# Optimization experiments

Hardware: AMD Instinct MI355X
Metric: run time of the kernel (lower is better)

Reference implementation:

```python
import jax, jax.numpy as jnp
import numpy as np

N_HEADS = 4
D_HEAD = 64
SCALE = D_HEAD ** -0.5


def setup_inputs() -> dict:
    key = jax.random.key(0)
    k0, k1, k2, k3, k4 = jax.random.split(key, 5)
    C = 256
    return {
        "x": jax.random.normal(k0, (32, C, 32, 32), dtype=jnp.float32),
        "W_qkv": jax.random.normal(k1, (C, 3 * N_HEADS * D_HEAD), dtype=jnp.float32) * 0.02,
        "b_qkv": jax.random.normal(k2, (3 * N_HEADS * D_HEAD,), dtype=jnp.float32) * 0.02,
        "W_out": jax.random.normal(k3, (C, C), dtype=jnp.float32) * 0.02,
        "b_out": jax.random.normal(k4, (C,), dtype=jnp.float32) * 0.02,
    }


def reference(x, W_qkv, b_qkv, W_out, b_out):
    b, c, h, w = x.shape
    # [B, C, H, W] -> [B, S, C], S = H*W  (NOTE: GroupNorm is defined in the
    # original module but never applied in forward; we match that exactly.)
    xs = x.reshape(b, c, h * w).transpose(0, 2, 1)
    qkv = (xs @ W_qkv + b_qkv).reshape(b, -1, N_HEADS, 3 * D_HEAD)
    q, k, v = jnp.split(qkv, 3, axis=-1)  # each [B, S, H, D]
    scores = jnp.einsum('bihd,bjhd->bijh', q, k) * SCALE  # [B, S, S, H]
    attn = jax.nn.softmax(scores, axis=2)  # softmax over key index j
    res = jnp.einsum('bijh,bjhd->bihd', attn, v).reshape(b, -1, N_HEADS * D_HEAD)
    res = res @ W_out + b_out + xs
    return res.transpose(0, 2, 1).reshape(b, c, h, w)
```

## Files before the change

### kernel.cpp

```cpp
#include <hip/hip_runtime.h>

#define NH 4
#define DH 64
#define SS 1024
#define CC 256

typedef __attribute__((ext_vector_type(8))) short short8;
typedef __attribute__((ext_vector_type(4))) float floatx4;
typedef __attribute__((ext_vector_type(16))) float floatx16;
typedef __attribute__((ext_vector_type(2))) unsigned uint2v;

#define MFMA16(a, b, c) __builtin_amdgcn_mfma_f32_16x16x32_bf16(a, b, c, 0, 0, 0)
#define MFMA32(a, b, c) __builtin_amdgcn_mfma_f32_32x32x16_bf16(a, b, c, 0, 0, 0)

#define QSCALE 0.18033688011112042f

__device__ __forceinline__ short f2bf(float f) {
    union { float f; unsigned u; } v; v.f = f;
    unsigned r = (v.u + 0x7fffu + ((v.u >> 16) & 1u)) >> 16;
    return (short)r;
}
__device__ __forceinline__ unsigned bfrn(float f) {
    union { float f; unsigned u; } v; v.f = f;
    return (v.u + 0x7fffu + ((v.u >> 16) & 1u)) >> 16;
}
__device__ __forceinline__ unsigned pk2_trunc(float a, float b) {
    union { float f; unsigned u; } ua, ub; ua.f = a; ub.f = b;
    return (ua.u >> 16) | (ub.u & 0xFFFF0000u);
}
__device__ __forceinline__ unsigned pk2_rn(float a, float b) {
    return bfrn(a) | (bfrn(b) << 16);
}

__global__ __launch_bounds__(256) void k_prep(const float* __restrict__ x,
                                              const float* __restrict__ Wqkv,
                                              const float* __restrict__ Wout,
                                              short* __restrict__ xs,
                                              short* __restrict__ Wqkv_t,
                                              short* __restrict__ Wout_t) {
    int bid = blockIdx.x;
    if (bid < 2048) {
        __shared__ float tile[64][65];
        int b = bid >> 6;
        int s0 = ((bid >> 2) & 15) * 64;
        int c0 = (bid & 3) * 64;
        int t = threadIdx.x;
        int tx = t & 63, ty = t >> 6;
        for (int i = 0; i < 16; ++i) {
            int c = ty + i * 4;
            tile[tx][c] = x[((b * CC) + (c0 + c)) * SS + s0 + tx];
        }
        __syncthreads();
        for (int i = 0; i < 8; ++i) {
            int s = (t >> 5) + i * 8;
            int cp = (t & 31) * 2;
            short2 v;
            v.x = f2bf(tile[s][cp]);
            v.y = f2bf(tile[s][cp + 1]);
            *(short2*)(&xs[((b * SS) + (s0 + s)) * CC + c0 + cp]) = v;
        }
    } else {
        int idx = (bid - 2048) * 256 + threadIdx.x;
        if (idx < 768 * 256) {
            int n = idx >> 8, k = idx & 255;
            Wqkv_t[idx] = f2bf(Wqkv[k * 768 + n]);
        } else {
            int j = idx - 768 * 256;
            int c = j >> 8, k = j & 255;
            Wout_t[j] = f2bf(Wout[k * 256 + c]);
        }
    }
}

__global__ __launch_bounds__(256) void k_qkv(const short* __restrict__ xs,
                                             const short* __restrict__ Wt,
                                             const float* __restrict__ bqkv,
                                             short* __restrict__ qtw,
                                             short* __restrict__ kw,
                                             short* __restrict__ vtw) {
    __shared__ short smem[10240];
    short* As = smem;
    short* Bs = smem + 5120;
    int bid = blockIdx.x;
    int idx = bid >> 3;
    int m0 = ((bid & 7) * 32 + idx / 6) * 128;
    int n0 = (idx % 6) * 128;
    int t = threadIdx.x;
    int lane = t & 63, wid = t >> 6;
    int wr = wid >> 1, wc = wid & 1;
    int c16 = lane & 15, qd = lane >> 4;

    floatx4 acc[4][4] = {};
    short8 pa[2], pb[2];

    for (int j = 0; j < 2; ++j) {
        int id = j * 256 + t, row = id >> 2, cc = id & 3;
        pa[j] = *(const short8*)(&xs[(m0 + row) * CC + cc * 8]);
        pb[j] = *(const short8*)(&Wt[(n0 + row) * CC + cc * 8]);
    }
    for (int kt = 0; kt < 8; ++kt) {
        if (kt) __syncthreads();
        for (int j = 0; j < 2; ++j) {
            int id = j * 256 + t, row = id >> 2, cc = id & 3;
            *(short8*)(&As[row * 40 + cc * 8]) = pa[j];
            *(short8*)(&Bs[row * 40 + cc * 8]) = pb[j];
        }
        __syncthreads();
        if (kt < 7) {
            for (int j = 0; j < 2; ++j) {
                int id = j * 256 + t, row = id >> 2, cc = id & 3;
                pa[j] = *(const short8*)(&xs[(m0 + row) * CC + (kt + 1) * 32 + cc * 8]);
                pb[j] = *(const short8*)(&Wt[(n0 + row) * CC + (kt + 1) * 32 + cc * 8]);
            }
        }
        short8 av[4], bv[4];
        for (int i = 0; i < 4; ++i) {
            av[i] = *(const short8*)(&As[(wr * 64 + i * 16 + c16) * 40 + qd * 8]);
            bv[i] = *(const short8*)(&Bs[(wc * 64 + i * 16 + c16) * 40 + qd * 8]);
        }
        for (int mi = 0; mi < 4; ++mi)
            for (int ni = 0; ni < 4; ++ni)
                acc[mi][ni] = MFMA16(av[mi], bv[ni], acc[mi][ni]);
    }

    int b = m0 >> 10, sbase = m0 & 1023;
    int seg = (n0 >> 6) + wc;
    float bias4[4];
    for (int ni = 0; ni < 4; ++ni)
        bias4[ni] = bqkv[n0 + wc * 64 + ni * 16 + c16];

    int seg0 = n0 >> 6;
    short* Tt = smem;
    for (int s2 = 0; s2 < 2; ++s2) {
        int sg = seg0 + s2;
        int type = sg % 3;
        if (type == 1) continue;
        float sc = (type == 0) ? QSCALE : 1.f;
        __syncthreads();
        if (wc == s2) {
            for (int mi = 0; mi < 4; ++mi)
                for (int ni = 0; ni < 4; ++ni)
                    for (int r = 0; r < 4; ++r)
                        Tt[(ni * 16 + c16) * 136 + wr * 64 + mi * 16 + qd * 4 + r] =
                            f2bf((acc[mi][ni][r] + bias4[ni]) * sc);
        }
        __syncthreads();
        short* dst = ((type == 0) ? qtw : vtw) + (size_t)((b * NH + sg / 3) * DH) * SS + sbase;
        for (int it = 0; it < 4; ++it) {
            int c = it * 256 + t;
            int d = c >> 4, off = (c & 15) * 8;
            *(short8*)(dst + (size_t)d * SS + off) =
                *(const short8*)(&Tt[d * 136 + off]);
        }
    }

    int kseg = (seg0 % 3 == 1) ? seg0 : (((seg0 + 1) % 3 == 1) ? seg0 + 1 : -1);
    if (kseg >= 0) {
        short* Kt = smem;
        __syncthreads();
        if (seg == kseg) {
            for (int mi = 0; mi < 4; ++mi)
                for (int ni = 0; ni < 4; ++ni)
                    for (int r = 0; r < 4; ++r)
                        Kt[(wr * 64 + mi * 16 + qd * 4 + r) * 72 + ni * 16 + c16] =
                            f2bf(acc[mi][ni][r] + bias4[ni]);
        }
        __syncthreads();
        int bhk = b * NH + kseg / 3;
        int srow = t >> 1, dh = (t & 1) * 32;
        short* gdst = &kw[(size_t)(bhk * SS + sbase + srow) * DH + dh];
        const short* lsrc = &Kt[srow * 72 + dh];
        for (int k = 0; k < 4; ++k)
            *(short8*)(gdst + k * 8) = *(const short8*)(lsrc + k * 8);
    }
}

__global__ __launch_bounds__(256) void k_attn(const short* __restrict__ qtw,
                                              const short* __restrict__ kw,
                                              const short* __restrict__ vtw,
                                              short* __restrict__ res) {
    __shared__ __align__(16) short Ks[2][64 * 72];
    __shared__ __align__(16) short Vts[2][64 * 72];
    int bid = blockIdx.x;
    int q0 = (bid >> 7) * 128;
    int bh = bid & 127;
    int t = threadIdx.x;
    int lane = t & 63, w = t >> 6;
    int l31 = lane & 31, hi = lane >> 5;
    const short* qp = qtw + (size_t)bh * DH * SS;
    const short* kp = kw + (size_t)bh * SS * DH;
    const short* vp = vtw + (size_t)bh * DH * SS;

    short8 qfrag[4];
    {
        int s = q0 + w * 32 + l31;
        for (int kd = 0; kd < 4; ++kd) {
            short8 q;
            for (int e = 0; e < 8; ++e)
                q[e] = qp[(size_t)(kd * 16 + hi * 8 + e) * SS + s];
            qfrag[kd] = q;
        }
    }

    float l_i = 0.f;
    floatx16 o_acc[2] = {};

    int srow0 = t >> 3, scc = (t & 7) * 8;
    int srow1 = srow0 + 32;
    short8 kreg[2], vreg[2];
    kreg[0] = *(const short8*)(&kp[srow0 * DH + scc]);
    vreg[0] = *(const short8*)(&vp[srow0 * SS + scc]);
    kreg[1] = *(const short8*)(&kp[srow1 * DH + scc]);
    vreg[1] = *(const short8*)(&vp[srow1 * SS + scc]);
    *(short8*)(&Ks[0][srow0 * 72 + scc]) = kreg[0];
    *(short8*)(&Vts[0][srow0 * 72 + scc]) = vreg[0];
    *(short8*)(&Ks[0][srow1 * 72 + scc]) = kreg[1];
    *(short8*)(&Vts[0][srow1 * 72 + scc]) = vreg[1];
    __syncthreads();

    int cur = 0;
    for (int kt = 0; kt < 16; ++kt) {
        if (kt < 15) {
            kreg[0] = *(const short8*)(&kp[((kt + 1) * 64 + srow0) * DH + scc]);
            vreg[0] = *(const short8*)(&vp[srow0 * SS + (kt + 1) * 64 + scc]);
            kreg[1] = *(const short8*)(&kp[((kt + 1) * 64 + srow1) * DH + scc]);
            vreg[1] = *(const short8*)(&vp[srow1 * SS + (kt + 1) * 64 + scc]);
        }

        const short* Kc = Ks[cur];
        const short* Vc = Vts[cur];
#pragma unroll
        for (int jt = 0; jt < 2; ++jt) {
            short8 kf[4];
#pragma unroll
            for (int kd = 0; kd < 4; ++kd)
                kf[kd] = *(const short8*)(&Kc[(jt * 32 + l31) * 72 + kd * 16 + hi * 8]);
            short8 vf0[2], vf1[2];
#pragma unroll
            for (int dt = 0; dt < 2; ++dt) {
                vf0[dt] = *(const short8*)(&Vc[(dt * 32 + l31) * 72 + (jt * 2 + 0) * 16 + hi * 8]);
                vf1[dt] = *(const short8*)(&Vc[(dt * 32 + l31) * 72 + (jt * 2 + 1) * 16 + hi * 8]);
            }

            floatx16 sacc = {};
            __builtin_amdgcn_s_setprio(1);
#pragma unroll
            for (int kd = 0; kd < 4; ++kd)
                sacc = MFMA32(kf[kd], qfrag[kd], sacc);
            __builtin_amdgcn_s_setprio(0);

            float ls = 0.f;
            unsigned u[8];
#pragma unroll
            for (int r = 0; r < 16; r += 2) {
                float e0 = __builtin_amdgcn_exp2f(sacc[r]);
                float e1 = __builtin_amdgcn_exp2f(sacc[r + 1]);
                ls += e0 + e1;
                u[r >> 1] = pk2_trunc(e0, e1);
            }
            l_i += ls;

            uint2v r02 = __builtin_amdgcn_permlane32_swap(u[0], u[2], false, false);
            uint2v r13 = __builtin_amdgcn_permlane32_swap(u[1], u[3], false, false);
            uint2v r46 = __builtin_amdgcn_permlane32_swap(u[4], u[6], false, false);
            uint2v r57 = __builtin_amdgcn_permlane32_swap(u[5], u[7], false, false);
            union { unsigned w[4]; short8 s; } pf0, pf1;
            pf0.w[0] = r02[0]; pf0.w[1] = r13[0]; pf0.w[2] = r02[1]; pf0.w[3] = r13[1];
            pf1.w[0] = r46[0]; pf1.w[1] = r57[0]; pf1.w[2] = r46[1]; pf1.w[3] = r57[1];

            __builtin_amdgcn_s_setprio(1);
#pragma unroll
            for (int dt = 0; dt < 2; ++dt) {
                o_acc[dt] = MFMA32(vf0[dt], pf0.s, o_acc[dt]);
                o_acc[dt] = MFMA32(vf1[dt], pf1.s, o_acc[dt]);
            }
            __builtin_amdgcn_s_setprio(0);
        }

        if (kt < 15) {
            *(short8*)(&Ks[cur ^ 1][srow0 * 72 + scc]) = kreg[0];
            *(short8*)(&Vts[cur ^ 1][srow0 * 72 + scc]) = vreg[0];
            *(short8*)(&Ks[cur ^ 1][srow1 * 72 + scc]) = kreg[1];
            *(short8*)(&Vts[cur ^ 1][srow1 * 72 + scc]) = vreg[1];
            __syncthreads();
            cur ^= 1;
        }
    }

    int b = bh >> 2, h = bh & 3;
    {
        float l = l_i;
        l += __shfl_xor(l, 32);
        float inv = 1.f / l;
        int s = q0 + w * 32 + l31;
        long base = (long)(b * SS + s) * CC + h * DH;
#pragma unroll
        for (int dt = 0; dt < 2; ++dt) {
#pragma unroll
            for (int q = 0; q < 4; ++q) {
                int d = dt * 32 + q * 8 + hi * 4;
                uint2 ow;
                ow.x = pk2_rn(o_acc[dt][q * 4 + 0] * inv, o_acc[dt][q * 4 + 1] * inv);
                ow.y = pk2_rn(o_acc[dt][q * 4 + 2] * inv, o_acc[dt][q * 4 + 3] * inv);
                *(uint2*)(&res[base + d]) = ow;
            }
        }
    }
}

__global__ __launch_bounds__(256) void k_out(const short* __restrict__ res,
                                             const short* __restrict__ Wot,
                                             const float* __restrict__ bout,
                                             const float* __restrict__ x,
                                             float* __restrict__ out) {
    __shared__ short As[2][64 * 40];
    __shared__ short Bs[2][128 * 40];
    int b = blockIdx.z;
    int m0 = blockIdx.y * 64;
    int n0 = blockIdx.x * 128;
    int t = threadIdx.x;
    int lane = t & 63, wid = t >> 6;
    int wr = wid >> 1, wc = wid & 1;
    int c16 = lane & 15, qd = lane >> 4;

    floatx4 acc[2][4] = {};
    int arow = t >> 2, ac4 = (t & 3) * 8;
    int brow0 = t >> 2, bc0 = (t & 3) * 8;
    int brow1 = brow0 + 64;
    short8 pa, pb0, pb1;
    pa  = *(const short8*)(&Wot[(m0 + arow) * CC + ac4]);
    pb0 = *(const short8*)(&res[(b * SS + n0 + brow0) * CC + bc0]);
    pb1 = *(const short8*)(&res[(b * SS + n0 + brow1) * CC + bc0]);
    *(short8*)(&As[0][arow * 40 + ac4]) = pa;
    *(short8*)(&Bs[0][brow0 * 40 + bc0]) = pb0;
    *(short8*)(&Bs[0][brow1 * 40 + bc0]) = pb1;
    __syncthreads();

    int cur = 0;
    for (int kt = 0; kt < 8; ++kt) {
        if (kt < 7) {
            pa  = *(const short8*)(&Wot[(m0 + arow) * CC + (kt + 1) * 32 + ac4]);
            pb0 = *(const short8*)(&res[(b * SS + n0 + brow0) * CC + (kt + 1) * 32 + bc0]);
            pb1 = *(const short8*)(&res[(b * SS + n0 + brow1) * CC + (kt + 1) * 32 + bc0]);
        }
        short8 av[2], bv[4];
        for (int i = 0; i < 2; ++i)
            av[i] = *(const short8*)(&As[cur][(wr * 32 + i * 16 + c16) * 40 + qd * 8]);
        for (int i = 0; i < 4; ++i)
            bv[i] = *(const short8*)(&Bs[cur][(wc * 64 + i * 16 + c16) * 40 + qd * 8]);
        for (int mi = 0; mi < 2; ++mi)
            for (int ni = 0; ni < 4; ++ni)
                acc[mi][ni] = MFMA16(av[mi], bv[ni], acc[mi][ni]);
        if (kt < 7) {
            *(short8*)(&As[cur ^ 1][arow * 40 + ac4]) = pa;
            *(short8*)(&Bs[cur ^ 1][brow0 * 40 + bc0]) = pb0;
            *(short8*)(&Bs[cur ^ 1][brow1 * 40 + bc0]) = pb1;
            __syncthreads();
            cur ^= 1;
        }
    }

    for (int mi = 0; mi < 2; ++mi) {
        for (int r = 0; r < 4; ++r) {
            int c = m0 + wr * 32 + mi * 16 + qd * 4 + r;
            float bias = bout[c];
            for (int ni = 0; ni < 4; ++ni) {
                int s = n0 + wc * 64 + ni * 16 + c16;
                float v = acc[mi][ni][r] + bias + x[((b * CC) + c) * SS + s];
                out[((b * CC) + c) * SS + s] = v;
            }
        }
    }
}

extern "C" void kernel_launch(void* const* d_in, const int* in_sizes, int n_in,
                              void* d_out, int out_size, void* d_ws, size_t ws_size,
                              hipStream_t stream) {
    const float* x    = (const float*)d_in[0];
    const float* Wqkv = (const float*)d_in[1];
    const float* bqkv = (const float*)d_in[2];
    const float* Wout = (const float*)d_in[3];
    const float* bout = (const float*)d_in[4];
    float* out = (float*)d_out;

    char* ws = (char*)d_ws;
    short* xs_res = (short*)(ws);
    short* qtw    = (short*)(ws + 16777216);
    short* kw     = (short*)(ws + 33554432);
    short* vtw    = (short*)(ws + 50331648);
    short* Wqkv_t = (short*)(ws + 67108864);
    short* Wout_t = (short*)(ws + 67502080);

    k_prep<<<dim3(3072), 256, 0, stream>>>(x, Wqkv, Wout, xs_res, Wqkv_t, Wout_t);
    k_qkv<<<dim3(1536), 256, 0, stream>>>(xs_res, Wqkv_t, bqkv, qtw, kw, vtw);
    k_attn<<<dim3(1024), 256, 0, stream>>>(qtw, kw, vtw, xs_res);
    k_out<<<dim3(8, 4, 32), 256, 0, stream>>>(xs_res, Wout_t, bout, x, out);
}
```

Before: 176.9 us.

## Use single-buffered 128-key tiles with register prefetch in attention kernel

The attention kernel's K/V staging changes from double-buffered 64-key LDS tiles to a single 128-key tile per iteration. The next tile is prefetched into registers and stored to LDS after a barrier. This halves the number of loop iterations and barriers and keeps LDS use about the same. In exchange it adds an extra barrier per iteration before overwriting the shared tile, and more registers hold the prefetched data, which may reduce occupancy.

```diff
diff --git a/kernel.cpp b/kernel.cpp
--- a/kernel.cpp
+++ b/kernel.cpp
@@ -179,8 +179,8 @@
                                               const short* __restrict__ kw,
                                               const short* __restrict__ vtw,
                                               short* __restrict__ res) {
-    __shared__ __align__(16) short Ks[2][64 * 72];
-    __shared__ __align__(16) short Vts[2][64 * 72];
+    __shared__ __align__(16) short Ks[128 * 72];
+    __shared__ __align__(16) short Vts[64 * 136];
     int bid = blockIdx.x;
     int q0 = (bid >> 7) * 128;
     int bh = bid & 127;
@@ -205,41 +205,46 @@
     float l_i = 0.f;
     floatx16 o_acc[2] = {};
 
-    int srow0 = t >> 3, scc = (t & 7) * 8;
-    int srow1 = srow0 + 32;
-    short8 kreg[2], vreg[2];
-    kreg[0] = *(const short8*)(&kp[srow0 * DH + scc]);
-    vreg[0] = *(const short8*)(&vp[srow0 * SS + scc]);
-    kreg[1] = *(const short8*)(&kp[srow1 * DH + scc]);
-    vreg[1] = *(const short8*)(&vp[srow1 * SS + scc]);
-    *(short8*)(&Ks[0][srow0 * 72 + scc]) = kreg[0];
-    *(short8*)(&Vts[0][srow0 * 72 + scc]) = vreg[0];
-    *(short8*)(&Ks[0][srow1 * 72 + scc]) = kreg[1];
-    *(short8*)(&Vts[0][srow1 * 72 + scc]) = vreg[1];
-    __syncthreads();
-
-    int cur = 0;
-    for (int kt = 0; kt < 16; ++kt) {
-        if (kt < 15) {
-            kreg[0] = *(const short8*)(&kp[((kt + 1) * 64 + srow0) * DH + scc]);
-            vreg[0] = *(const short8*)(&vp[srow0 * SS + (kt + 1) * 64 + scc]);
-            kreg[1] = *(const short8*)(&kp[((kt + 1) * 64 + srow1) * DH + scc]);
-            vreg[1] = *(const short8*)(&vp[srow1 * SS + (kt + 1) * 64 + scc]);
-        }
-
-        const short* Kc = Ks[cur];
-        const short* Vc = Vts[cur];
-#pragma unroll
-        for (int jt = 0; jt < 2; ++jt) {
+    short8 kreg[4], vreg[4];
+    for (int j = 0; j < 4; ++j) {
+        int L = j * 256 + t;
+        int kr = L >> 3, kc = (L & 7) * 8;
+        kreg[j] = *(const short8*)(&kp[kr * DH + kc]);
+        int vd = L >> 4, vc = (L & 15) * 8;
+        vreg[j] = *(const short8*)(&vp[vd * SS + vc]);
+    }
+
+    for (int kt = 0; kt < 8; ++kt) {
+        if (kt) __syncthreads();
+        for (int j = 0; j < 4; ++j) {
+            int L = j * 256 + t;
+            int kr = L >> 3, kc = (L & 7) * 8;
+            *(short8*)(&Ks[kr * 72 + kc]) = kreg[j];
+            int vd = L >> 4, vc = (L & 15) * 8;
+            *(short8*)(&Vts[vd * 136 + vc]) = vreg[j];
+        }
+        __syncthreads();
+        if (kt < 7) {
+            for (int j = 0; j < 4; ++j) {
+                int L = j * 256 + t;
+                int kr = L >> 3, kc = (L & 7) * 8;
+                kreg[j] = *(const short8*)(&kp[((kt + 1) * 128 + kr) * DH + kc]);
+                int vd = L >> 4, vc = (L & 15) * 8;
+                vreg[j] = *(const short8*)(&vp[vd * SS + (kt + 1) * 128 + vc]);
+            }
+        }
+
+#pragma unroll
+        for (int jt = 0; jt < 4; ++jt) {
             short8 kf[4];
 #pragma unroll
             for (int kd = 0; kd < 4; ++kd)
-                kf[kd] = *(const short8*)(&Kc[(jt * 32 + l31) * 72 + kd * 16 + hi * 8]);
+                kf[kd] = *(const short8*)(&Ks[(jt * 32 + l31) * 72 + kd * 16 + hi * 8]);
             short8 vf0[2], vf1[2];
 #pragma unroll
             for (int dt = 0; dt < 2; ++dt) {
-                vf0[dt] = *(const short8*)(&Vc[(dt * 32 + l31) * 72 + (jt * 2 + 0) * 16 + hi * 8]);
-                vf1[dt] = *(const short8*)(&Vc[(dt * 32 + l31) * 72 + (jt * 2 + 1) * 16 + hi * 8]);
+                vf0[dt] = *(const short8*)(&Vts[(dt * 32 + l31) * 136 + (jt * 2 + 0) * 16 + hi * 8]);
+                vf1[dt] = *(const short8*)(&Vts[(dt * 32 + l31) * 136 + (jt * 2 + 1) * 16 + hi * 8]);
             }
 
             floatx16 sacc = {};
@@ -275,15 +280,6 @@
                 o_acc[dt] = MFMA32(vf1[dt], pf1.s, o_acc[dt]);
             }
             __builtin_amdgcn_s_setprio(0);
-        }
-
-        if (kt < 15) {
-            *(short8*)(&Ks[cur ^ 1][srow0 * 72 + scc]) = kreg[0];
-            *(short8*)(&Vts[cur ^ 1][srow0 * 72 + scc]) = vreg[0];
-            *(short8*)(&Ks[cur ^ 1][srow1 * 72 + scc]) = kreg[1];
-            *(short8*)(&Vts[cur ^ 1][srow1 * 72 + scc]) = vreg[1];
-            __syncthreads();
-            cur ^= 1;
         }
     }
 
```

New measurement: 179.2 us. About the same (+1.3%).
